# Kernel optimization log

Measured on AMD Instinct MI355X. Metric: run time of the kernel, lower is better.

Reference implementation:

```python
import jax, jax.numpy as jnp
import numpy as np

N, S, D, H = 2048, 16, 128, 8
EPS = 1e-5  # torch.nn.LayerNorm default eps


def setup_inputs() -> dict:
    key = jax.random.key(0)
    ks = jax.random.split(key, 3)
    return {
        "x": jax.random.normal(ks[0], (N, S, D), jnp.float32),
        "Wi": jax.random.normal(ks[1], (H, S, D, D), jnp.float32),
        "Wj": jax.random.normal(ks[2], (H, S, 2 * D, D), jnp.float32),
        "ln1_w": jnp.ones((S, D), jnp.float32),
        "ln1_b": jnp.zeros((S, D), jnp.float32),
        "prelu1_a": jnp.float32(0.25),  # torch PReLU default single param
        "ln2_w": jnp.ones((H, D), jnp.float32),
        "ln2_b": jnp.zeros((H, D), jnp.float32),
        "prelu2_a": jnp.float32(0.25),
    }


def _layernorm2(x, w, b):
    # LayerNorm over the last two dims (matches torch LayerNorm([A, B]))
    mu = jnp.mean(x, axis=(-2, -1), keepdims=True)
    var = jnp.var(x, axis=(-2, -1), keepdims=True)
    return (x - mu) * jax.lax.rsqrt(var + EPS) * w + b


def _prelu(x, a):
    return jnp.where(x >= 0, x, a * x)


def reference(x, Wi, Wj, ln1_w, ln1_b, prelu1_a, ln2_w, ln2_b, prelu2_a):
    n, s, d = x.shape
    h = Wi.shape[0]
    # sort descending along source dim
    idx = jnp.argsort(-x, axis=1)                      # [N,S,D] int
    x_sort = jnp.take_along_axis(x, idx, axis=1)       # [N,S,D]
    # pad with a zero row, take adjacent differences
    pad = jnp.concatenate([x_sort, jnp.zeros((n, 1, d), x.dtype)], axis=1)
    diff = pad[:, :-1, :] - pad[:, 1:, :]              # [N,S,D]
    # positional encoding: cumsum of 2^rank / 2^S
    enc = jnp.cumsum(jnp.exp2(idx.astype(x.dtype)), axis=1) / jnp.asarray(2.0 ** s, x.dtype)
    # per-head, per-source batched matmul with Wi
    se = jnp.einsum('bsd,hsdo->bhso', enc, Wi)         # [N,H,S,D]
    se = _prelu(_layernorm2(se, ln1_w, ln1_b), prelu1_a)  # Dropout in eval mode = identity
    cat = jnp.concatenate(
        [jnp.broadcast_to(diff[:, None, :, :], (n, h, s, d)), se], axis=-1
    )                                                  # [N,H,S,2D]
    out = jnp.einsum('bhsd,hsdo->bho', cat, Wj)        # [N,H,D]
    return _prelu(_layernorm2(out, ln2_w, ln2_b), prelu2_a)
```

## Files before the change

kernel.cpp:

```cpp
#include <hip/hip_runtime.h>

#define N_ 2048
#define S_ 16
#define D_ 128
#define H_ 8
#define EPS_ 1e-5f

typedef unsigned short ushortT;
typedef unsigned int uint32;
typedef __attribute__((ext_vector_type(8))) short short8;
typedef __attribute__((ext_vector_type(8))) unsigned short ushort8;
typedef __attribute__((ext_vector_type(4))) float f32x4;
typedef __attribute__((ext_vector_type(4))) unsigned int uint4v;
typedef __attribute__((ext_vector_type(8))) float float8;

__device__ __forceinline__ ushortT f2bf(float f) {
  union { float f; uint32 u; } c; c.f = f;
  uint32 u = c.u;
  u = (u + 0x7FFFu + ((u >> 16) & 1u)) >> 16;
  return (ushortT)u;
}
__device__ __forceinline__ float bf2f(ushortT b) {
  union { uint32 u; float f; } c; c.u = ((uint32)b) << 16;
  return c.f;
}

__global__ __launch_bounds__(256) void k_prep(const float* __restrict__ x,
                                              ushortT* __restrict__ enc,
                                              ushortT* __restrict__ diff) {
  int g = blockIdx.x * 256 + threadIdx.x;
  int n = g >> 7, d = g & 127;
  const float* xp = x + (size_t)n * (S_ * D_) + d;
  float v[S_];
#pragma unroll
  for (int s = 0; s < S_; ++s) v[s] = xp[s * D_];
  int r[S_];
#pragma unroll
  for (int i = 0; i < S_; ++i) {
    int ri = 0;
#pragma unroll
    for (int j = 0; j < S_; ++j)
      ri += ((v[j] > v[i]) || (v[j] == v[i] && j < i)) ? 1 : 0;
    r[i] = ri;
  }
  float xs[S_ + 1];
#pragma unroll
  for (int s = 0; s < S_; ++s) {
    float acc = 0.f;
#pragma unroll
    for (int i = 0; i < S_; ++i) acc += (r[i] == s) ? v[i] : 0.f;
    xs[s] = acc;
  }
  xs[S_] = 0.f;
  ushortT* ep = enc + (size_t)n * (S_ * D_) + d;
  ushortT* dp = diff + (size_t)n * (S_ * D_) + d;
#pragma unroll
  for (int s = 0; s < S_; ++s) {
    uint32 mm = 0;
#pragma unroll
    for (int i = 0; i < S_; ++i) mm |= (r[i] <= s) ? (1u << i) : 0u;
    ep[s * D_] = f2bf((float)mm * (1.f / 65536.f));
    dp[s * D_] = f2bf(xs[s] - xs[s + 1]);
  }
}

__global__ __launch_bounds__(256) void k_castWi(const float* __restrict__ Wi,
                                                ushortT* __restrict__ Wit) {
  __shared__ ushortT tile[D_ * 136];
  int hs = blockIdx.x;
  const float* src = Wi + (size_t)hs * D_ * D_;
  int t = threadIdx.x;
#pragma unroll 4
  for (int i = 0; i < 64; ++i) {
    int e = t + 256 * i;
    int dd = e >> 7, o = e & 127;
    tile[dd * 136 + o] = f2bf(src[e]);
  }
  __syncthreads();
  int o = t >> 1, dbase = (t & 1) * 64;
  ushortT* dst = Wit + ((size_t)hs * D_ + o) * D_ + dbase;
#pragma unroll
  for (int c = 0; c < 8; ++c) {
    uint4v pk;
#pragma unroll
    for (int q = 0; q < 4; ++q) {
      ushortT lo = tile[(dbase + c * 8 + q * 2) * 136 + o];
      ushortT hi = tile[(dbase + c * 8 + q * 2 + 1) * 136 + o];
      pk[q] = (uint32)lo | ((uint32)hi << 16);
    }
    *(uint4v*)(dst + c * 8) = pk;
  }
}

__global__ __launch_bounds__(256) void k_castWj(const float* __restrict__ Wj,
                                                ushortT* __restrict__ Wjt) {
  __shared__ ushortT tile[128 * 136];
  int hs = blockIdx.x; int h = hs >> 4, s = hs & 15;
  const float* src = Wj + (size_t)hs * 256 * D_;
  int t = threadIdx.x;
  for (int half = 0; half < 2; ++half) {
#pragma unroll 4
    for (int i = 0; i < 64; ++i) {
      int e = t + 256 * i;
      int dd = e >> 7, o = e & 127;
      tile[dd * 136 + o] = f2bf(src[half * 16384 + e]);
    }
    __syncthreads();
    int o = t >> 1, db = (t & 1) * 64;
    ushortT* dst = Wjt + ((size_t)(h * D_ + o)) * (S_ * 256) + s * 256 + half * 128 + db;
#pragma unroll
    for (int c = 0; c < 8; ++c) {
      uint4v pk;
#pragma unroll
      for (int q = 0; q < 4; ++q) {
        ushortT lo = tile[(db + c * 8 + q * 2) * 136 + o];
        ushortT hi = tile[(db + c * 8 + q * 2 + 1) * 136 + o];
        pk[q] = (uint32)lo | ((uint32)hi << 16);
      }
      *(uint4v*)(dst + c * 8) = pk;
    }
    __syncthreads();
  }
}

__global__ __launch_bounds__(256) void k_gemm1(const ushortT* __restrict__ enc,
                                               const ushortT* __restrict__ Wit,
                                               ushortT* __restrict__ se,
                                               float* __restrict__ ssum,
                                               float* __restrict__ ssq) {
  int bt = blockIdx.x, s = blockIdx.y, h = blockIdx.z;
  __shared__ ushortT As[128 * 128];
  __shared__ ushortT Bs[128 * 128];
  int tid = threadIdx.x;
#pragma unroll
  for (int i = 0; i < 8; ++i) {
    int c = tid + 256 * i;
    int row = c >> 4, c16 = c & 15;
    int sw = ((c16 ^ (row & 7)) * 8);
    uint4v va = *(const uint4v*)(enc + (size_t)(bt * 128 + row) * (S_ * D_) + s * D_ + c16 * 8);
    *(uint4v*)(As + row * 128 + sw) = va;
    uint4v vb = *(const uint4v*)(Wit + ((size_t)((h * S_ + s) * D_) + row) * D_ + c16 * 8);
    *(uint4v*)(Bs + row * 128 + sw) = vb;
  }
  __syncthreads();
  int wave = tid >> 6, lane = tid & 63;
  int l15 = lane & 15, lg = lane >> 4;
  f32x4 acc[2][8];
#pragma unroll
  for (int i = 0; i < 2; ++i)
#pragma unroll
    for (int j = 0; j < 8; ++j) acc[i][j] = (f32x4)(0.f);
#pragma unroll
  for (int kk = 0; kk < 4; ++kk) {
    int cc = kk * 4 + lg;
    short8 a[2], b[8];
#pragma unroll
    for (int i = 0; i < 2; ++i) {
      int row = wave * 32 + i * 16 + l15;
      a[i] = *(const short8*)(As + row * 128 + ((cc ^ (row & 7)) * 8));
    }
#pragma unroll
    for (int j = 0; j < 8; ++j) {
      int row = j * 16 + l15;
      b[j] = *(const short8*)(Bs + row * 128 + ((cc ^ (row & 7)) * 8));
    }
#pragma unroll
    for (int i = 0; i < 2; ++i)
#pragma unroll
      for (int j = 0; j < 8; ++j)
        acc[i][j] = __builtin_amdgcn_mfma_f32_16x16x32_bf16(a[i], b[j], acc[i][j], 0, 0, 0);
  }
#pragma unroll
  for (int i = 0; i < 2; ++i) {
#pragma unroll
    for (int rr = 0; rr < 4; ++rr) {
      int rloc = wave * 32 + i * 16 + lg * 4 + rr;
      int b_g = bt * 128 + rloc;
      float rs = 0.f, rq = 0.f;
#pragma unroll
      for (int j = 0; j < 8; ++j) {
        float val = acc[i][j][rr];
        rs += val; rq += val * val;
      }
#pragma unroll
      for (int m = 1; m <= 8; m <<= 1) {
        rs += __shfl_xor(rs, m);
        rq += __shfl_xor(rq, m);
      }
      if (l15 == 0) {
        ssum[((size_t)s * N_ + b_g) * H_ + h] = rs;
        ssq[((size_t)s * N_ + b_g) * H_ + h] = rq;
      }
    }
  }
  __syncthreads();
#pragma unroll
  for (int i = 0; i < 2; ++i)
#pragma unroll
    for (int rr = 0; rr < 4; ++rr) {
      int row = wave * 32 + i * 16 + lg * 4 + rr;
      int sw = (row & 7) << 3;
#pragma unroll
      for (int j = 0; j < 8; ++j) {
        int o = j * 16 + l15;
        As[row * 128 + (o ^ sw)] = f2bf(acc[i][j][rr]);
      }
    }
  __syncthreads();
#pragma unroll
  for (int p = 0; p < 2; ++p) {
    int row = p * 64 + (tid >> 2);
    int sw = (row & 7) << 3;
    int b_g = bt * 128 + row;
    ushortT* dst = se + (((size_t)b_g * H_ + h) * S_ + s) * D_;
#pragma unroll
    for (int q = 0; q < 4; ++q) {
      int o0 = (q * 4 + (tid & 3)) * 8;
      *(uint4v*)(dst + o0) = *(const uint4v*)(As + row * 128 + (o0 ^ sw));
    }
  }
}

__global__ __launch_bounds__(256) void k_finalize(const float* __restrict__ ssum,
                                                  const float* __restrict__ ssq,
                                                  float* __restrict__ mr) {
  int t = blockIdx.x * 256 + threadIdx.x;
  float s1 = 0.f, s2 = 0.f;
#pragma unroll
  for (int s = 0; s < S_; ++s) {
    s1 += ssum[(size_t)s * (N_ * H_) + t];
    s2 += ssq[(size_t)s * (N_ * H_) + t];
  }
  float mu = s1 * (1.f / 2048.f);
  float var = s2 * (1.f / 2048.f) - mu * mu;
  mr[t * 2] = mu;
  mr[t * 2 + 1] = rsqrtf(var + EPS_);
}

__global__ __launch_bounds__(256) void k_act(ushortT* __restrict__ se,
                                             const float* __restrict__ mr,
                                             const float* __restrict__ ln1w,
                                             const float* __restrict__ ln1b,
                                             const float* __restrict__ pa1) {
  int g = blockIdx.x * 256 + threadIdx.x;
  int d8 = g & 15, s = (g >> 4) & 15, bh = g >> 8;
  float mu = mr[bh * 2], rstd = mr[bh * 2 + 1];
  float a1 = pa1[0];
  ushort8 v = *(ushort8*)(se + (size_t)g * 8);
  float8 w = *(const float8*)(ln1w + s * D_ + d8 * 8);
  float8 bb = *(const float8*)(ln1b + s * D_ + d8 * 8);
  ushort8 r;
#pragma unroll
  for (int e = 0; e < 8; ++e) {
    float f = bf2f(v[e]);
    float y = (f - mu) * rstd * w[e] + bb[e];
    y = (y >= 0.f) ? y : a1 * y;
    r[e] = f2bf(y);
  }
  *(ushort8*)(se + (size_t)g * 8) = r;
}

__global__ __launch_bounds__(256, 3) void k_gemm2(const ushortT* __restrict__ diff,
                                                  const ushortT* __restrict__ se,
                                                  const ushortT* __restrict__ Wjt,
                                                  float* __restrict__ outp,
                                                  int scount) {
  int bt = blockIdx.x, sh = blockIdx.y, h = blockIdx.z;
  int s0 = sh * scount;
  __shared__ ushortT As[128 * 64];
  __shared__ ushortT Bs[128 * 64];
  int tid = threadIdx.x;
  int c8 = tid & 7, trow = tid >> 3;
  int swst = ((c8 ^ (trow & 7)) * 8);
  int wave = tid >> 6, lane = tid & 63;
  int l15 = lane & 15, lg = lane >> 4;
  int wm = wave >> 1, wn = wave & 1;

  uint32 aoff_d[4], aoff_s[4], boff[4];
#pragma unroll
  for (int i = 0; i < 4; ++i) {
    int row = i * 32 + trow;
    aoff_d[i] = (uint32)(bt * 128 + row) * (S_ * D_) + c8 * 8;
    aoff_s[i] = ((uint32)(bt * 128 + row) * H_ + h) * (S_ * D_) + c8 * 8;
    boff[i] = (uint32)(h * D_ + row) * (S_ * 256) + c8 * 8;
  }
  uint4v ra[4], rb[4];
  int nc = scount * 4;
  {
    uint32 add = s0 * D_;
#pragma unroll
    for (int i = 0; i < 4; ++i) {
      ra[i] = *(const uint4v*)(diff + aoff_d[i] + add);
      rb[i] = *(const uint4v*)(Wjt + boff[i] + s0 * 256);
    }
  }
  f32x4 acc[4][4];
#pragma unroll
  for (int i = 0; i < 4; ++i)
#pragma unroll
    for (int j = 0; j < 4; ++j) acc[i][j] = (f32x4)(0.f);

  for (int c = 0; c < nc; ++c) {
    if (c) __syncthreads();
#pragma unroll
    for (int i = 0; i < 4; ++i) {
      int row = i * 32 + trow;
      *(uint4v*)(As + row * 64 + swst) = ra[i];
      *(uint4v*)(Bs + row * 64 + swst) = rb[i];
    }
    if (c + 1 < nc) {
      int cn = c + 1;
      int s = s0 + (cn >> 2), p = cn & 3;
      uint32 add = s * D_ + (p & 1) * 64;
      uint32 badd = s * 256 + p * 64;
#pragma unroll
      for (int i = 0; i < 4; ++i) {
        ra[i] = (p < 2) ? *(const uint4v*)(diff + aoff_d[i] + add)
                        : *(const uint4v*)(se + aoff_s[i] + add);
        rb[i] = *(const uint4v*)(Wjt + boff[i] + badd);
      }
    }
    __syncthreads();
#pragma unroll
    for (int kk = 0; kk < 2; ++kk) {
      int cc = kk * 4 + lg;
      short8 a[4], b[4];
#pragma unroll
      for (int i = 0; i < 4; ++i) {
        int row = wm * 64 + i * 16 + l15;
        a[i] = *(const short8*)(As + row * 64 + ((cc ^ (row & 7)) * 8));
      }
#pragma unroll
      for (int j = 0; j < 4; ++j) {
        int row = wn * 64 + j * 16 + l15;
        b[j] = *(const short8*)(Bs + row * 64 + ((cc ^ (row & 7)) * 8));
      }
#pragma unroll
      for (int i = 0; i < 4; ++i)
#pragma unroll
        for (int j = 0; j < 4; ++j)
          acc[i][j] = __builtin_amdgcn_mfma_f32_16x16x32_bf16(a[i], b[j], acc[i][j], 0, 0, 0);
    }
  }
#pragma unroll
  for (int i = 0; i < 4; ++i)
#pragma unroll
    for (int j = 0; j < 4; ++j)
#pragma unroll
      for (int rr = 0; rr < 4; ++rr) {
        int b_g = bt * 128 + wm * 64 + i * 16 + lg * 4 + rr;
        int o = wn * 64 + j * 16 + l15;
        outp[(((size_t)sh * N_ + b_g) * H_ + h) * D_ + o] = acc[i][j][rr];
      }
}

__global__ __launch_bounds__(256) void k_ln2(const float* __restrict__ outp,
                                             const float* __restrict__ ln2w,
                                             const float* __restrict__ ln2b,
                                             const float* __restrict__ pa2,
                                             float* __restrict__ out,
                                             int nsplit) {
  int b = blockIdx.x, t = threadIdx.x;
  __shared__ float red[8];
  __shared__ float stats[2];
  f32x4 v = (f32x4)(0.f);
  for (int p = 0; p < nsplit; ++p)
    v += *((const f32x4*)(outp + (size_t)p * (N_ * 1024) + (size_t)b * 1024) + t);
  float s1 = v[0] + v[1] + v[2] + v[3];
  float s2 = v[0] * v[0] + v[1] * v[1] + v[2] * v[2] + v[3] * v[3];
#pragma unroll
  for (int m = 1; m <= 32; m <<= 1) {
    s1 += __shfl_xor(s1, m);
    s2 += __shfl_xor(s2, m);
  }
  int wave = t >> 6, lane = t & 63;
  if (lane == 0) { red[wave] = s1; red[4 + wave] = s2; }
  __syncthreads();
  if (t == 0) {
    float S = red[0] + red[1] + red[2] + red[3];
    float Q = red[4] + red[5] + red[6] + red[7];
    float mu = S * (1.f / 1024.f);
    float var = Q * (1.f / 1024.f) - mu * mu;
    stats[0] = mu; stats[1] = rsqrtf(var + EPS_);
  }
  __syncthreads();
  float mu = stats[0], rstd = stats[1];
  float a2 = pa2[0];
  f32x4 wv = *((const f32x4*)ln2w + t);
  f32x4 bv = *((const f32x4*)ln2b + t);
  f32x4 r;
#pragma unroll
  for (int e = 0; e < 4; ++e) {
    float y = (v[e] - mu) * rstd * wv[e] + bv[e];
    r[e] = (y >= 0.f) ? y : a2 * y;
  }
  *((f32x4*)(out + (size_t)b * 1024) + t) = r;
}

extern "C" void kernel_launch(void* const* d_in, const int* in_sizes, int n_in,
                              void* d_out, int out_size, void* d_ws, size_t ws_size,
                              hipStream_t stream) {
  const float* x    = (const float*)d_in[0];
  const float* Wi   = (const float*)d_in[1];
  const float* Wj   = (const float*)d_in[2];
  const float* ln1w = (const float*)d_in[3];
  const float* ln1b = (const float*)d_in[4];
  const float* pa1  = (const float*)d_in[5];
  const float* ln2w = (const float*)d_in[6];
  const float* ln2b = (const float*)d_in[7];
  const float* pa2  = (const float*)d_in[8];
  char* ws = (char*)d_ws;
  ushortT* se   = (ushortT*)(ws + 0);
  ushortT* diff = (ushortT*)(ws + 67108864);
  ushortT* Wjt  = (ushortT*)(ws + 75497472);
  float*   outp = (float*)(ws + 83886080);
  ushortT* enc  = (ushortT*)(ws + 83886080);
  ushortT* Wit  = (ushortT*)(ws + 92274688);
  float*   ssum = (float*)(ws + 96468992);
  float*   ssq  = (float*)(ws + 97517568);
  float*   mr   = (float*)(ws + 98566144);
  float*   out  = (float*)d_out;

  int nsplit = (ws_size >= 117440512ull) ? 4 : 2;
  int scount = S_ / nsplit;

  hipLaunchKernelGGL(k_prep, dim3(1024), dim3(256), 0, stream, x, enc, diff);
  hipLaunchKernelGGL(k_castWi, dim3(128), dim3(256), 0, stream, Wi, Wit);
  hipLaunchKernelGGL(k_castWj, dim3(128), dim3(256), 0, stream, Wj, Wjt);
  hipLaunchKernelGGL(k_gemm1, dim3(16, 16, 8), dim3(256), 0, stream, enc, Wit, se, ssum, ssq);
  hipLaunchKernelGGL(k_finalize, dim3(64), dim3(256), 0, stream, ssum, ssq, mr);
  hipLaunchKernelGGL(k_act, dim3(16384), dim3(256), 0, stream, se, mr, ln1w, ln1b, pa1);
  hipLaunchKernelGGL(k_gemm2, dim3(16, nsplit, 8), dim3(256), 0, stream, diff, se, Wjt, outp, scount);
  hipLaunchKernelGGL(k_ln2, dim3(2048), dim3(256), 0, stream, outp, ln2w, ln2b, pa2, out, nsplit);
}
```

Before: 217.7 us.

## Fuse LN1+PReLU into gemm2 load, reuse enc tile across heads, merge weight casts

Removes the separate k_act pass, which read and rewrote the whole 64MB bf16 se tensor. LayerNorm1 and PReLU are now applied on the fly to se tiles as k_gemm2 stages them into shared memory. k_gemm1 keeps the enc A-fragments in registers and loops over 4 heads per block, prefetching the next head's Wi tile while the current one computes. The two weight-cast kernels are merged into one launch. The costs are more register pressure in both GEMMs, fewer gemm1 blocks, and relocating mr so it does not overlap outp.

```diff
diff --git a/kernel.cpp b/kernel.cpp
--- a/kernel.cpp
+++ b/kernel.cpp
@@ -64,62 +64,62 @@
   }
 }
 
-__global__ __launch_bounds__(256) void k_castWi(const float* __restrict__ Wi,
-                                                ushortT* __restrict__ Wit) {
-  __shared__ ushortT tile[D_ * 136];
-  int hs = blockIdx.x;
-  const float* src = Wi + (size_t)hs * D_ * D_;
+__global__ __launch_bounds__(256) void k_castW(const float* __restrict__ Wi,
+                                               const float* __restrict__ Wj,
+                                               ushortT* __restrict__ Wit,
+                                               ushortT* __restrict__ Wjt) {
+  __shared__ ushortT tile[128 * 136];
+  int bx = blockIdx.x;
   int t = threadIdx.x;
-#pragma unroll 4
-  for (int i = 0; i < 64; ++i) {
-    int e = t + 256 * i;
-    int dd = e >> 7, o = e & 127;
-    tile[dd * 136 + o] = f2bf(src[e]);
-  }
-  __syncthreads();
-  int o = t >> 1, dbase = (t & 1) * 64;
-  ushortT* dst = Wit + ((size_t)hs * D_ + o) * D_ + dbase;
-#pragma unroll
-  for (int c = 0; c < 8; ++c) {
-    uint4v pk;
-#pragma unroll
-    for (int q = 0; q < 4; ++q) {
-      ushortT lo = tile[(dbase + c * 8 + q * 2) * 136 + o];
-      ushortT hi = tile[(dbase + c * 8 + q * 2 + 1) * 136 + o];
-      pk[q] = (uint32)lo | ((uint32)hi << 16);
-    }
-    *(uint4v*)(dst + c * 8) = pk;
-  }
-}
-
-__global__ __launch_bounds__(256) void k_castWj(const float* __restrict__ Wj,
-                                                ushortT* __restrict__ Wjt) {
-  __shared__ ushortT tile[128 * 136];
-  int hs = blockIdx.x; int h = hs >> 4, s = hs & 15;
-  const float* src = Wj + (size_t)hs * 256 * D_;
-  int t = threadIdx.x;
-  for (int half = 0; half < 2; ++half) {
+  if (bx < 128) {
+    int hs = bx;
+    const float* src = Wi + (size_t)hs * D_ * D_;
 #pragma unroll 4
     for (int i = 0; i < 64; ++i) {
       int e = t + 256 * i;
       int dd = e >> 7, o = e & 127;
-      tile[dd * 136 + o] = f2bf(src[half * 16384 + e]);
+      tile[dd * 136 + o] = f2bf(src[e]);
     }
     __syncthreads();
-    int o = t >> 1, db = (t & 1) * 64;
-    ushortT* dst = Wjt + ((size_t)(h * D_ + o)) * (S_ * 256) + s * 256 + half * 128 + db;
+    int o = t >> 1, dbase = (t & 1) * 64;
+    ushortT* dst = Wit + ((size_t)hs * D_ + o) * D_ + dbase;
 #pragma unroll
     for (int c = 0; c < 8; ++c) {
       uint4v pk;
 #pragma unroll
       for (int q = 0; q < 4; ++q) {
-        ushortT lo = tile[(db + c * 8 + q * 2) * 136 + o];
-        ushortT hi = tile[(db + c * 8 + q * 2 + 1) * 136 + o];
+        ushortT lo = tile[(dbase + c * 8 + q * 2) * 136 + o];
+        ushortT hi = tile[(dbase + c * 8 + q * 2 + 1) * 136 + o];
         pk[q] = (uint32)lo | ((uint32)hi << 16);
       }
       *(uint4v*)(dst + c * 8) = pk;
     }
-    __syncthreads();
+  } else {
+    int hs = bx - 128; int h = hs >> 4, s = hs & 15;
+    const float* src = Wj + (size_t)hs * 256 * D_;
+    for (int half = 0; half < 2; ++half) {
+      if (half) __syncthreads();
+#pragma unroll 4
+      for (int i = 0; i < 64; ++i) {
+        int e = t + 256 * i;
+        int dd = e >> 7, o = e & 127;
+        tile[dd * 136 + o] = f2bf(src[half * 16384 + e]);
+      }
+      __syncthreads();
+      int o = t >> 1, db = (t & 1) * 64;
+      ushortT* dst = Wjt + ((size_t)(h * D_ + o)) * (S_ * 256) + s * 256 + half * 128 + db;
+#pragma unroll
+      for (int c = 0; c < 8; ++c) {
+        uint4v pk;
+#pragma unroll
+        for (int q = 0; q < 4; ++q) {
+          ushortT lo = tile[(db + c * 8 + q * 2) * 136 + o];
+          ushortT hi = tile[(db + c * 8 + q * 2 + 1) * 136 + o];
+          pk[q] = (uint32)lo | ((uint32)hi << 16);
+        }
+        *(uint4v*)(dst + c * 8) = pk;
+      }
+    }
   }
 }
 
@@ -128,95 +128,118 @@
                                                ushortT* __restrict__ se,
                                                float* __restrict__ ssum,
                                                float* __restrict__ ssq) {
-  int bt = blockIdx.x, s = blockIdx.y, h = blockIdx.z;
+  int bt = blockIdx.x, s = blockIdx.y, hp = blockIdx.z;
+  int h0 = hp * 4;
   __shared__ ushortT As[128 * 128];
   __shared__ ushortT Bs[128 * 128];
   int tid = threadIdx.x;
-#pragma unroll
-  for (int i = 0; i < 8; ++i) {
-    int c = tid + 256 * i;
-    int row = c >> 4, c16 = c & 15;
-    int sw = ((c16 ^ (row & 7)) * 8);
-    uint4v va = *(const uint4v*)(enc + (size_t)(bt * 128 + row) * (S_ * D_) + s * D_ + c16 * 8);
-    *(uint4v*)(As + row * 128 + sw) = va;
-    uint4v vb = *(const uint4v*)(Wit + ((size_t)((h * S_ + s) * D_) + row) * D_ + c16 * 8);
-    *(uint4v*)(Bs + row * 128 + sw) = vb;
-  }
-  __syncthreads();
+  int c16 = tid & 15, prow = tid >> 4;
   int wave = tid >> 6, lane = tid & 63;
   int l15 = lane & 15, lg = lane >> 4;
-  f32x4 acc[2][8];
-#pragma unroll
-  for (int i = 0; i < 2; ++i)
-#pragma unroll
-    for (int j = 0; j < 8; ++j) acc[i][j] = (f32x4)(0.f);
-#pragma unroll
-  for (int kk = 0; kk < 4; ++kk) {
-    int cc = kk * 4 + lg;
-    short8 a[2], b[8];
+
+  ushort8 rb[8];
+#pragma unroll
+  for (int i = 0; i < 8; ++i) {
+    int row = prow + 16 * i;
+    int sw = ((c16 ^ (row & 7)) * 8);
+    ushort8 va = *(const ushort8*)(enc + (size_t)(bt * 128 + row) * (S_ * D_) + s * D_ + c16 * 8);
+    *(ushort8*)(As + row * 128 + sw) = va;
+    rb[i] = *(const ushort8*)(Wit + ((size_t)((h0 * S_ + s) * D_) + row) * D_ + c16 * 8);
+  }
+  __syncthreads();
+  short8 afr[4][2];
+#pragma unroll
+  for (int kk = 0; kk < 4; ++kk)
 #pragma unroll
     for (int i = 0; i < 2; ++i) {
       int row = wave * 32 + i * 16 + l15;
-      a[i] = *(const short8*)(As + row * 128 + ((cc ^ (row & 7)) * 8));
-    }
-#pragma unroll
-    for (int j = 0; j < 8; ++j) {
-      int row = j * 16 + l15;
-      b[j] = *(const short8*)(Bs + row * 128 + ((cc ^ (row & 7)) * 8));
-    }
+      int cc = kk * 4 + lg;
+      afr[kk][i] = *(const short8*)(As + row * 128 + ((cc ^ (row & 7)) * 8));
+    }
+
+  for (int hh = 0; hh < 4; ++hh) {
+    int h = h0 + hh;
+    if (hh) __syncthreads();
+#pragma unroll
+    for (int i = 0; i < 8; ++i) {
+      int row = prow + 16 * i;
+      *(ushort8*)(Bs + row * 128 + ((c16 ^ (row & 7)) * 8)) = rb[i];
+    }
+    if (hh < 3) {
+#pragma unroll
+      for (int i = 0; i < 8; ++i) {
+        int row = prow + 16 * i;
+        rb[i] = *(const ushort8*)(Wit + ((size_t)(((h + 1) * S_ + s) * D_) + row) * D_ + c16 * 8);
+      }
+    }
+    __syncthreads();
+    f32x4 acc[2][8];
 #pragma unroll
     for (int i = 0; i < 2; ++i)
 #pragma unroll
-      for (int j = 0; j < 8; ++j)
-        acc[i][j] = __builtin_amdgcn_mfma_f32_16x16x32_bf16(a[i], b[j], acc[i][j], 0, 0, 0);
-  }
-#pragma unroll
-  for (int i = 0; i < 2; ++i) {
-#pragma unroll
-    for (int rr = 0; rr < 4; ++rr) {
-      int rloc = wave * 32 + i * 16 + lg * 4 + rr;
-      int b_g = bt * 128 + rloc;
-      float rs = 0.f, rq = 0.f;
+      for (int j = 0; j < 8; ++j) acc[i][j] = (f32x4)(0.f);
+#pragma unroll
+    for (int kk = 0; kk < 4; ++kk) {
+      int cc = kk * 4 + lg;
+      short8 b[8];
 #pragma unroll
       for (int j = 0; j < 8; ++j) {
-        float val = acc[i][j][rr];
-        rs += val; rq += val * val;
-      }
-#pragma unroll
-      for (int m = 1; m <= 8; m <<= 1) {
-        rs += __shfl_xor(rs, m);
-        rq += __shfl_xor(rq, m);
-      }
-      if (l15 == 0) {
-        ssum[((size_t)s * N_ + b_g) * H_ + h] = rs;
-        ssq[((size_t)s * N_ + b_g) * H_ + h] = rq;
-      }
-    }
-  }
-  __syncthreads();
-#pragma unroll
-  for (int i = 0; i < 2; ++i)
-#pragma unroll
-    for (int rr = 0; rr < 4; ++rr) {
-      int row = wave * 32 + i * 16 + lg * 4 + rr;
+        int row = j * 16 + l15;
+        b[j] = *(const short8*)(Bs + row * 128 + ((cc ^ (row & 7)) * 8));
+      }
+#pragma unroll
+      for (int i = 0; i < 2; ++i)
+#pragma unroll
+        for (int j = 0; j < 8; ++j)
+          acc[i][j] = __builtin_amdgcn_mfma_f32_16x16x32_bf16(afr[kk][i], b[j], acc[i][j], 0, 0, 0);
+    }
+#pragma unroll
+    for (int i = 0; i < 2; ++i)
+#pragma unroll
+      for (int rr = 0; rr < 4; ++rr) {
+        int rloc = wave * 32 + i * 16 + lg * 4 + rr;
+        int b_g = bt * 128 + rloc;
+        float rs = 0.f, rq = 0.f;
+#pragma unroll
+        for (int j = 0; j < 8; ++j) {
+          float val = acc[i][j][rr];
+          rs += val; rq += val * val;
+        }
+#pragma unroll
+        for (int m = 1; m <= 8; m <<= 1) {
+          rs += __shfl_xor(rs, m);
+          rq += __shfl_xor(rq, m);
+        }
+        if (l15 == 0) {
+          ssum[((size_t)s * N_ + b_g) * H_ + h] = rs;
+          ssq[((size_t)s * N_ + b_g) * H_ + h] = rq;
+        }
+      }
+    __syncthreads();
+#pragma unroll
+    for (int i = 0; i < 2; ++i)
+#pragma unroll
+      for (int rr = 0; rr < 4; ++rr) {
+        int row = wave * 32 + i * 16 + lg * 4 + rr;
+        int sw = (row & 7) << 3;
+#pragma unroll
+        for (int j = 0; j < 8; ++j) {
+          int o = j * 16 + l15;
+          Bs[row * 128 + (o ^ sw)] = f2bf(acc[i][j][rr]);
+        }
+      }
+    __syncthreads();
+#pragma unroll
+    for (int p = 0; p < 2; ++p) {
+      int row = p * 64 + (tid >> 2);
       int sw = (row & 7) << 3;
-#pragma unroll
-      for (int j = 0; j < 8; ++j) {
-        int o = j * 16 + l15;
-        As[row * 128 + (o ^ sw)] = f2bf(acc[i][j][rr]);
-      }
-    }
-  __syncthreads();
-#pragma unroll
-  for (int p = 0; p < 2; ++p) {
-    int row = p * 64 + (tid >> 2);
-    int sw = (row & 7) << 3;
-    int b_g = bt * 128 + row;
-    ushortT* dst = se + (((size_t)b_g * H_ + h) * S_ + s) * D_;
-#pragma unroll
-    for (int q = 0; q < 4; ++q) {
-      int o0 = (q * 4 + (tid & 3)) * 8;
-      *(uint4v*)(dst + o0) = *(const uint4v*)(As + row * 128 + (o0 ^ sw));
+      int b_g = bt * 128 + row;
+      ushortT* dst = se + (((size_t)b_g * H_ + h) * S_ + s) * D_;
+#pragma unroll
+      for (int q = 0; q < 4; ++q) {
+        int o0 = (q * 4 + (tid & 3)) * 8;
+        *(uint4v*)(dst + o0) = *(const uint4v*)(Bs + row * 128 + (o0 ^ sw));
+      }
     }
   }
 }
@@ -237,32 +260,13 @@
   mr[t * 2 + 1] = rsqrtf(var + EPS_);
 }
 
-__global__ __launch_bounds__(256) void k_act(ushortT* __restrict__ se,
-                                             const float* __restrict__ mr,
-                                             const float* __restrict__ ln1w,
-                                             const float* __restrict__ ln1b,
-                                             const float* __restrict__ pa1) {
-  int g = blockIdx.x * 256 + threadIdx.x;
-  int d8 = g & 15, s = (g >> 4) & 15, bh = g >> 8;
-  float mu = mr[bh * 2], rstd = mr[bh * 2 + 1];
-  float a1 = pa1[0];
-  ushort8 v = *(ushort8*)(se + (size_t)g * 8);
-  float8 w = *(const float8*)(ln1w + s * D_ + d8 * 8);
-  float8 bb = *(const float8*)(ln1b + s * D_ + d8 * 8);
-  ushort8 r;
-#pragma unroll
-  for (int e = 0; e < 8; ++e) {
-    float f = bf2f(v[e]);
-    float y = (f - mu) * rstd * w[e] + bb[e];
-    y = (y >= 0.f) ? y : a1 * y;
-    r[e] = f2bf(y);
-  }
-  *(ushort8*)(se + (size_t)g * 8) = r;
-}
-
 __global__ __launch_bounds__(256, 3) void k_gemm2(const ushortT* __restrict__ diff,
                                                   const ushortT* __restrict__ se,
                                                   const ushortT* __restrict__ Wjt,
+                                                  const float* __restrict__ mr,
+                                                  const float* __restrict__ ln1w,
+                                                  const float* __restrict__ ln1b,
+                                                  const float* __restrict__ pa1,
                                                   float* __restrict__ outp,
                                                   int scount) {
   int bt = blockIdx.x, sh = blockIdx.y, h = blockIdx.z;
@@ -275,23 +279,28 @@
   int wave = tid >> 6, lane = tid & 63;
   int l15 = lane & 15, lg = lane >> 4;
   int wm = wave >> 1, wn = wave & 1;
-
+  float a1 = pa1[0];
+
+  float mu_r[4], rs_r[4];
   uint32 aoff_d[4], aoff_s[4], boff[4];
 #pragma unroll
   for (int i = 0; i < 4; ++i) {
     int row = i * 32 + trow;
-    aoff_d[i] = (uint32)(bt * 128 + row) * (S_ * D_) + c8 * 8;
-    aoff_s[i] = ((uint32)(bt * 128 + row) * H_ + h) * (S_ * D_) + c8 * 8;
+    int b_g = bt * 128 + row;
+    mu_r[i] = mr[((size_t)b_g * H_ + h) * 2];
+    rs_r[i] = mr[((size_t)b_g * H_ + h) * 2 + 1];
+    aoff_d[i] = (uint32)b_g * (S_ * D_) + c8 * 8;
+    aoff_s[i] = ((uint32)b_g * H_ + h) * (S_ * D_) + c8 * 8;
     boff[i] = (uint32)(h * D_ + row) * (S_ * 256) + c8 * 8;
   }
-  uint4v ra[4], rb[4];
+  ushort8 ra[4], rb[4];
   int nc = scount * 4;
   {
     uint32 add = s0 * D_;
 #pragma unroll
     for (int i = 0; i < 4; ++i) {
-      ra[i] = *(const uint4v*)(diff + aoff_d[i] + add);
-      rb[i] = *(const uint4v*)(Wjt + boff[i] + s0 * 256);
+      ra[i] = *(const ushort8*)(diff + aoff_d[i] + add);
+      rb[i] = *(const ushort8*)(Wjt + boff[i] + s0 * 256);
     }
   }
   f32x4 acc[4][4];
@@ -301,23 +310,40 @@
     for (int j = 0; j < 4; ++j) acc[i][j] = (f32x4)(0.f);
 
   for (int c = 0; c < nc; ++c) {
+    int p = c & 3, s = s0 + (c >> 2);
     if (c) __syncthreads();
+    if (p >= 2) {
+      float8 w8 = *(const float8*)(ln1w + s * D_ + (p & 1) * 64 + c8 * 8);
+      float8 b8 = *(const float8*)(ln1b + s * D_ + (p & 1) * 64 + c8 * 8);
+#pragma unroll
+      for (int i = 0; i < 4; ++i) {
+        ushort8 v = ra[i];
+#pragma unroll
+        for (int e = 0; e < 8; ++e) {
+          float f = bf2f(v[e]);
+          float y = (f - mu_r[i]) * rs_r[i] * w8[e] + b8[e];
+          y = (y >= 0.f) ? y : a1 * y;
+          v[e] = f2bf(y);
+        }
+        ra[i] = v;
+      }
+    }
 #pragma unroll
     for (int i = 0; i < 4; ++i) {
       int row = i * 32 + trow;
-      *(uint4v*)(As + row * 64 + swst) = ra[i];
-      *(uint4v*)(Bs + row * 64 + swst) = rb[i];
+      *(ushort8*)(As + row * 64 + swst) = ra[i];
+      *(ushort8*)(Bs + row * 64 + swst) = rb[i];
     }
     if (c + 1 < nc) {
       int cn = c + 1;
-      int s = s0 + (cn >> 2), p = cn & 3;
-      uint32 add = s * D_ + (p & 1) * 64;
-      uint32 badd = s * 256 + p * 64;
+      int sn = s0 + (cn >> 2), pn = cn & 3;
+      uint32 add = sn * D_ + (pn & 1) * 64;
+      uint32 badd = sn * 256 + pn * 64;
 #pragma unroll
       for (int i = 0; i < 4; ++i) {
-        ra[i] = (p < 2) ? *(const uint4v*)(diff + aoff_d[i] + add)
-                        : *(const uint4v*)(se + aoff_s[i] + add);
-        rb[i] = *(const uint4v*)(Wjt + boff[i] + badd);
+        ra[i] = (pn < 2) ? *(const ushort8*)(diff + aoff_d[i] + add)
+                         : *(const ushort8*)(se + aoff_s[i] + add);
+        rb[i] = *(const ushort8*)(Wjt + boff[i] + badd);
       }
     }
     __syncthreads();
@@ -418,18 +444,17 @@
   ushortT* Wit  = (ushortT*)(ws + 92274688);
   float*   ssum = (float*)(ws + 96468992);
   float*   ssq  = (float*)(ws + 97517568);
-  float*   mr   = (float*)(ws + 98566144);
   float*   out  = (float*)d_out;
 
-  int nsplit = (ws_size >= 117440512ull) ? 4 : 2;
+  int nsplit = (ws_size >= 117571584ull) ? 4 : 2;
   int scount = S_ / nsplit;
+  float* mr = (float*)(ws + 83886080 + (size_t)nsplit * 8388608);
 
   hipLaunchKernelGGL(k_prep, dim3(1024), dim3(256), 0, stream, x, enc, diff);
-  hipLaunchKernelGGL(k_castWi, dim3(128), dim3(256), 0, stream, Wi, Wit);
-  hipLaunchKernelGGL(k_castWj, dim3(128), dim3(256), 0, stream, Wj, Wjt);
-  hipLaunchKernelGGL(k_gemm1, dim3(16, 16, 8), dim3(256), 0, stream, enc, Wit, se, ssum, ssq);
+  hipLaunchKernelGGL(k_castW, dim3(256), dim3(256), 0, stream, Wi, Wj, Wit, Wjt);
+  hipLaunchKernelGGL(k_gemm1, dim3(16, 16, 2), dim3(256), 0, stream, enc, Wit, se, ssum, ssq);
   hipLaunchKernelGGL(k_finalize, dim3(64), dim3(256), 0, stream, ssum, ssq, mr);
-  hipLaunchKernelGGL(k_act, dim3(16384), dim3(256), 0, stream, se, mr, ln1w, ln1b, pa1);
-  hipLaunchKernelGGL(k_gemm2, dim3(16, nsplit, 8), dim3(256), 0, stream, diff, se, Wjt, outp, scount);
+  hipLaunchKernelGGL(k_gemm2, dim3(16, nsplit, 8), dim3(256), 0, stream, diff, se, Wjt, mr,
+                     ln1w, ln1b, pa1, outp, scount);
   hipLaunchKernelGGL(k_ln2, dim3(2048), dim3(256), 0, stream, outp, ln2w, ln2b, pa2, out, nsplit);
 }
```

Result: faster. 208.1 us (-4.4%).
